# Optimization experiments

Measured on AMD Instinct MI355X. Metric: run time of the kernel, lower is better.

Reference implementation:

```python
import jax, jax.numpy as jnp
import numpy as np

B, TED, G, N, E, MD, NOISE = 10000, 512, 64, 2000, 64000, 15, 128
PAC = 10
PACDIM = (TED + NOISE) * PAC  # 6400
D0, D1 = 1024, 512


def _linear_params(k, fan_in, fan_out):
    kw, kb = jax.random.split(k)
    lim = 1.0 / np.sqrt(fan_in)
    w = jax.random.uniform(kw, (fan_in, fan_out), minval=-lim, maxval=lim, dtype=jnp.float32)
    b = jax.random.uniform(kb, (fan_out,), minval=-lim, maxval=lim, dtype=jnp.float32)
    return w, b


def setup_inputs() -> dict:
    key = jax.random.key(0)
    ks = jax.random.split(key, 12)
    inp = {
        'input_': jax.random.normal(ks[0], (B, TED), dtype=jnp.float32),
        'graphs_x': jax.random.normal(ks[1], (G, N, 1), dtype=jnp.float32),
        'edge_index': jax.random.randint(ks[2], (G, 2, E), 0, N, dtype=jnp.int32),
        'graph_ids': jax.random.randint(ks[3], (B,), 0, G, dtype=jnp.int32),
        'chain': jax.random.normal(ks[4], (B, 1), dtype=jnp.float32),
        'metadata': jax.random.normal(ks[5], (B, MD), dtype=jnp.float32),
    }
    inp['gcn_w'], inp['gcn_b'] = _linear_params(ks[6], 1, 1)
    inp['meta_w'], inp['meta_b'] = _linear_params(ks[7], 1 + MD, 32)
    inp['gme_w'], inp['gme_b'] = _linear_params(ks[8], N + 32, NOISE)
    inp['seq_w0'], inp['seq_b0'] = _linear_params(ks[9], PACDIM, D0)
    inp['seq_w1'], inp['seq_b1'] = _linear_params(ks[10], D0, D1)
    inp['seq_w2'], inp['seq_b2'] = _linear_params(ks[11], D1, 1)
    return inp


def _gcn_one(x, ei, gcn_w, gcn_b):
    # GCNConv(1,1) with self-loops and symmetric normalization.
    loops = jnp.arange(N, dtype=ei.dtype)
    src = jnp.concatenate([ei[0], loops])
    dst = jnp.concatenate([ei[1], loops])
    deg = jax.ops.segment_sum(jnp.ones_like(src, dtype=x.dtype), dst, num_segments=N)
    dinv = jax.lax.rsqrt(deg)  # deg >= 1 due to self-loops
    norm = dinv[src] * dinv[dst]  # [E+N]
    xw = x @ gcn_w  # [N,1]
    msg = xw[src] * norm[:, None]
    out = jax.ops.segment_sum(msg, dst, num_segments=N) + gcn_b
    return out.reshape(-1)  # flatten -> [N]


def reference(input_, graphs_x, edge_index, graph_ids, chain, metadata,
              gcn_w, gcn_b, meta_w, meta_b, gme_w, gme_b,
              seq_w0, seq_b0, seq_w1, seq_b1, seq_w2, seq_b2):
    # per-unique-graph GCN, vectorized over G graphs
    gcn_out = jax.vmap(lambda x, ei: _gcn_one(x, ei, gcn_w, gcn_b))(graphs_x, edge_index)  # [G,N]
    graph_emb = gcn_out[graph_ids]  # gather: [B,N]
    all_meta = jnp.concatenate([chain, metadata], axis=1)  # [B,1+MD]
    meta_emb = jax.nn.relu(all_meta @ meta_w + meta_b)  # [B,32]
    noise = jnp.concatenate([graph_emb, meta_emb], axis=1) @ gme_w + gme_b  # [B,NOISE]
    h = jnp.concatenate([input_, noise], axis=1).reshape(-1, PACDIM)  # [B/PAC, PACDIM]
    h = jax.nn.leaky_relu(h @ seq_w0 + seq_b0, 0.2)  # dropout omitted (eval mode)
    h = jax.nn.leaky_relu(h @ seq_w1 + seq_b1, 0.2)
    return h @ seq_w2 + seq_b2  # [B/PAC, 1]
```

## Files before the change

### kernel.cpp

```cpp
#include <hip/hip_runtime.h>

typedef __bf16 bf16_t;
typedef __bf16 bf16x4 __attribute__((ext_vector_type(4)));
typedef __bf16 bf16x8 __attribute__((ext_vector_type(8)));
typedef float floatx4 __attribute__((ext_vector_type(4)));

#define G_GRAPHS 64
#define N_NODES 2000
#define N_EDGES 64000
#define BATCH 10000
#define TED_ 512
#define NOISE_ 128
#define PACDIM_ 6400
#define D0_ 1024
#define D1_ 512
#define MROWS 1000
#define ESPLIT 8
#define EPB (N_EDGES / ESPLIT)
#define MSPLIT 8
#define EPB_MSG (N_EDGES / MSPLIT)
#define S0 8

#define DEG_BLKS 512
#define PACK_BLKS 1250
#define W0T_BLKS 6400
#define W1T_BLKS 512

__device__ __forceinline__ void glds16(const void* g, void* l) {
    __builtin_amdgcn_global_load_lds(
        (__attribute__((address_space(1))) void*)(g),
        (__attribute__((address_space(3))) void*)(l), 16, 0, 0);
}

__global__ __launch_bounds__(256) void prep_kernel(
    const int* __restrict__ edge_index, float* __restrict__ degs_part,
    const float* __restrict__ in, bf16_t* __restrict__ A,
    const float* __restrict__ W0, bf16_t* __restrict__ W0t,
    const float* __restrict__ W1, bf16_t* __restrict__ W1t)
{
    __shared__ float h[N_NODES];
    __shared__ float t[32][33];
    const int b = blockIdx.x, tid = threadIdx.x;
    if (b < DEG_BLKS) {
        const int s = b & 7, g = b >> 3;
        for (int n = tid; n < N_NODES; n += 256) h[n] = 0.f;
        __syncthreads();
        const int4* d4 = (const int4*)(edge_index + (size_t)g * 2 * N_EDGES
                                       + N_EDGES + s * EPB);
        for (int e = tid; e < EPB / 4; e += 256) {
            int4 v = d4[e];
            atomicAdd(&h[v.x], 1.0f); atomicAdd(&h[v.y], 1.0f);
            atomicAdd(&h[v.z], 1.0f); atomicAdd(&h[v.w], 1.0f);
        }
        __syncthreads();
        float* dp = degs_part + ((size_t)g * ESPLIT + s) * N_NODES;
        for (int n = tid; n < N_NODES; n += 256) dp[n] = h[n];
        return;
    }
    if (b < DEG_BLKS + PACK_BLKS) {
        int base = (b - DEG_BLKS) * 1024;
        for (int u = 0; u < 4; u++) {
            int idx = base + u * 256 + tid;
            float4 v = ((const float4*)in)[idx];
            int bb = idx >> 7;
            int c = (idx & 127) << 2;
            int r = bb / 10, slot = bb - r * 10;
            bf16x4 o = { (bf16_t)v.x, (bf16_t)v.y, (bf16_t)v.z, (bf16_t)v.w };
            *(bf16x4*)(A + (size_t)r * PACDIM_ + slot * 640 + c) = o;
        }
        return;
    }
    const float* W; bf16_t* Wt; int Rr, Cc, c0, r0;
    if (b < DEG_BLKS + PACK_BLKS + W0T_BLKS) {
        int tile = b - (DEG_BLKS + PACK_BLKS);
        W = W0; Wt = W0t; Rr = PACDIM_; Cc = D0_;
        c0 = (tile & 31) << 5; r0 = (tile >> 5) << 5;
    } else {
        int tile = b - (DEG_BLKS + PACK_BLKS + W0T_BLKS);
        W = W1; Wt = W1t; Rr = D0_; Cc = D1_;
        c0 = (tile & 15) << 5; r0 = (tile >> 4) << 5;
    }
    int tx = tid & 31, ty = tid >> 5;
    for (int yy = ty; yy < 32; yy += 8)
        t[yy][tx] = W[(size_t)(r0 + yy) * Cc + c0 + tx];
    __syncthreads();
    for (int yy = ty; yy < 32; yy += 8)
        Wt[(size_t)(c0 + yy) * Rr + r0 + tx] = (bf16_t)t[tx][yy];
}

__global__ __launch_bounds__(512) void msg_kernel(
    const float* __restrict__ graphs_x, const int* __restrict__ edge_index,
    const float* __restrict__ degs_part, float* __restrict__ outs_part)
{
    __shared__ float ys[N_NODES];
    __shared__ float dvl[N_NODES];
    __shared__ float oh[N_NODES];
    const int g = blockIdx.y, s = blockIdx.x, tid = threadIdx.x;
    const float* xg = graphs_x + (size_t)g * N_NODES;
    const float* dgp = degs_part + (size_t)g * ESPLIT * N_NODES;
    for (int n = tid; n < N_NODES; n += 512) {
        float d = 1.0f;
        for (int p = 0; p < ESPLIT; p++) d += dgp[(size_t)p * N_NODES + n];
        float dv = rsqrtf(d);
        dvl[n] = dv;
        ys[n] = xg[n] * dv;
        oh[n] = 0.f;
    }
    __syncthreads();
    const int* src = edge_index + (size_t)g * 2 * N_EDGES + s * EPB_MSG;
    const int2* s2 = (const int2*)src;
    const int2* d2 = (const int2*)(src + N_EDGES);
    for (int e = tid; e < EPB_MSG / 2; e += 512) {
        int2 sv = s2[e], dd = d2[e];
        atomicAdd(&oh[dd.x], ys[sv.x] * dvl[dd.x]);
        atomicAdd(&oh[dd.y], ys[sv.y] * dvl[dd.y]);
    }
    __syncthreads();
    float* op = outs_part + ((size_t)g * MSPLIT + s) * N_NODES;
    for (int n = tid; n < N_NODES; n += 512) op[n] = oh[n];
}

__global__ __launch_bounds__(512) void gnoise_kernel(
    const float* __restrict__ graphs_x, const float* __restrict__ degs_part,
    const float* __restrict__ outs_part,
    const float* __restrict__ gcn_w, const float* __restrict__ gcn_b,
    const float* __restrict__ gme_w, float* __restrict__ gnoise_p)
{
    __shared__ float of[500];
    __shared__ float part[4][128];
    const int s = blockIdx.x, g = blockIdx.y, tid = threadIdx.x;
    const int nBase = s * 500;
    const float w = gcn_w[0], bb = gcn_b[0];
    const float* dgp = degs_part + (size_t)g * ESPLIT * N_NODES;
    const float* otp = outs_part + (size_t)g * MSPLIT * N_NODES;
    for (int n = tid; n < 500; n += 512) {
        int gn = nBase + n;
        float d = 1.0f, o = 0.f;
        for (int p = 0; p < ESPLIT; p++) d += dgp[(size_t)p * N_NODES + gn];
        for (int p = 0; p < MSPLIT; p++) o += otp[(size_t)p * N_NODES + gn];
        of[n] = w * (o + graphs_x[(size_t)g * N_NODES + gn] / d) + bb;
    }
    __syncthreads();
    const int j = tid & 127, ch = tid >> 7;
    float acc = 0.f;
    const int n0 = ch * 125;
    for (int n = n0; n < n0 + 125; n++)
        acc += of[n] * gme_w[(size_t)(nBase + n) * 128 + j];
    part[ch][j] = acc;
    __syncthreads();
    if (tid < 128)
        gnoise_p[((size_t)g * 4 + s) * 128 + tid] =
            part[0][tid] + part[1][tid] + part[2][tid] + part[3][tid];
}

__global__ __launch_bounds__(256) void meta_kernel(
    const float* __restrict__ chain, const float* __restrict__ metadata,
    const int* __restrict__ graph_ids,
    const float* __restrict__ meta_w, const float* __restrict__ meta_b,
    const float* __restrict__ gme_w, const float* __restrict__ gme_b,
    const float* __restrict__ gnoise_p, bf16_t* __restrict__ A)
{
    int wid = (blockIdx.x * 256 + threadIdx.x) >> 6;
    int lane = threadIdx.x & 63;
    if (wid >= BATCH) return;
    const int b = wid;
    float me = 0.f;
    if (lane < 32) {
        me = meta_b[lane] + chain[b] * meta_w[lane];
        for (int i = 1; i < 16; i++)
            me += metadata[(size_t)b * 15 + (i - 1)] * meta_w[(size_t)i * 32 + lane];
        me = me > 0.f ? me : 0.f;
    }
    const int gid = graph_ids[b];
    const float* gp = gnoise_p + (size_t)gid * 4 * 128;
    const int j1 = lane, j2 = lane + 64;
    float n1 = gme_b[j1] + gp[j1] + gp[128 + j1] + gp[256 + j1] + gp[384 + j1];
    float n2 = gme_b[j2] + gp[j2] + gp[128 + j2] + gp[256 + j2] + gp[384 + j2];
    for (int k = 0; k < 32; k++) {
        float mk = __shfl(me, k, 64);
        const float* wrow = gme_w + (size_t)(N_NODES + k) * 128;
        n1 += mk * wrow[j1];
        n2 += mk * wrow[j2];
    }
    int r = b / 10, slot = b - r * 10;
    bf16_t* dp = A + (size_t)r * PACDIM_ + slot * 640 + TED_;
    dp[j1] = (bf16_t)n1;
    dp[j2] = (bf16_t)n2;
}

__global__ __launch_bounds__(256) void gemm_bt_splitk_kernel(
    const bf16_t* __restrict__ A,
    const bf16_t* __restrict__ Bt,
    float* __restrict__ P,
    int M, int N, int K, int KS, int zbits, int xbits, int Mp)
{
    __shared__ __align__(16) bf16_t As[2][128 * 32];
    __shared__ __align__(16) bf16_t Bs[2][128 * 32];
    const int tid = threadIdx.x;
    const int wave = tid >> 6;
    const int lane = tid & 63;
    const int id = blockIdx.x;
    const int z = id & ((1 << zbits) - 1);
    const int xt = (id >> zbits) & ((1 << xbits) - 1);
    const int yt = id >> (zbits + xbits);
    const int mBase = yt * 128;
    const int nBase = xt * 128;
    const int wm = (wave & 1) * 64;
    const int wn = (wave >> 1) * 64;

    floatx4 acc[4][4] = {};

    const int rA0 = tid >> 2;
    const int g4 = tid & 3;
    const int f4 = (rA0 >> 1) & 3;
    const int k8 = (g4 ^ f4) * 8;
    int gm0 = mBase + rA0;      if (gm0 > M - 1) gm0 = M - 1;
    int gm1 = mBase + 64 + rA0; if (gm1 > M - 1) gm1 = M - 1;
    const bf16_t* aP0 = A + (size_t)gm0 * K + k8;
    const bf16_t* aP1 = A + (size_t)gm1 * K + k8;
    const bf16_t* bP0 = Bt + (size_t)(nBase + rA0) * K + k8;
    const bf16_t* bP1 = Bt + (size_t)(nBase + 64 + rA0) * K + k8;

    const int q4 = lane >> 4;
    const int mr = lane & 15;
    const int kq = ((q4 ^ ((mr >> 1) & 3)) * 8);
    int aOff[4], bOff[4];
    for (int i = 0; i < 4; i++) aOff[i] = (wm + i * 16 + mr) * 32 + kq;
    for (int j = 0; j < 4; j++) bOff[j] = (wn + j * 16 + mr) * 32 + kq;

    const int nIter = KS >> 5;
    const int kc = z * KS;
    {
        char* lA = (char*)(&As[0][0]) + wave * 1024;
        char* lB = (char*)(&Bs[0][0]) + wave * 1024;
        glds16(aP0 + kc, lA);
        glds16(aP1 + kc, lA + 4096);
        glds16(bP0 + kc, lB);
        glds16(bP1 + kc, lB + 4096);
    }
    __syncthreads();
    for (int t = 0; t < nIter; ++t) {
        const int cur = t & 1;
        if (t + 1 < nIter) {
            const int kn = kc + (t + 1) * 32;
            char* lA = (char*)(&As[cur ^ 1][0]) + wave * 1024;
            char* lB = (char*)(&Bs[cur ^ 1][0]) + wave * 1024;
            glds16(aP0 + kn, lA);
            glds16(aP1 + kn, lA + 4096);
            glds16(bP0 + kn, lB);
            glds16(bP1 + kn, lB + 4096);
        }
        const bf16_t* aB = &As[cur][0];
        const bf16_t* bB = &Bs[cur][0];
        bf16x8 af[4], bfr[4];
        for (int i = 0; i < 4; i++) af[i] = *(const bf16x8*)(aB + aOff[i]);
        for (int j = 0; j < 4; j++) bfr[j] = *(const bf16x8*)(bB + bOff[j]);
        for (int i = 0; i < 4; i++)
            for (int j = 0; j < 4; j++)
                acc[i][j] = __builtin_amdgcn_mfma_f32_16x16x32_bf16(
                    af[i], bfr[j], acc[i][j], 0, 0, 0);
        __syncthreads();
    }

    float* Pz = P + (size_t)z * Mp * N;
    const int rq = (lane >> 4) * 4;
    const int cn = lane & 15;
    for (int j = 0; j < 4; j++) {
        int col = nBase + wn + j * 16 + cn;
        for (int i = 0; i < 4; i++)
            for (int r = 0; r < 4; r++) {
                int rowm = mBase + wm + i * 16 + rq + r;
                Pz[(size_t)rowm * N + col] = acc[i][j][r];
            }
    }
}

__global__ __launch_bounds__(256) void reduce_bias_leaky_kernel(
    const float* __restrict__ P, const float* __restrict__ bias,
    bf16_t* __restrict__ C, int M, int N, int Mp, int S,
    const float* __restrict__ b2, float* __restrict__ outp)
{
    if (blockIdx.x == 0 && threadIdx.x < MROWS / 4) {
        float bb2 = b2[0];
        ((float4*)outp)[threadIdx.x] = make_float4(bb2, bb2, bb2, bb2);
    }
    int idx = blockIdx.x * 256 + threadIdx.x;
    int total = M * (N >> 2);
    if (idx >= total) return;
    int nv = N >> 2;
    int r = idx / nv, c4 = (idx - r * nv) << 2;
    size_t off = (size_t)r * N + c4;
    size_t stride = (size_t)Mp * N;
    float4 v = *(const float4*)(P + off);
    for (int s = 1; s < S; s++) {
        float4 u = *(const float4*)(P + s * stride + off);
        v.x += u.x; v.y += u.y; v.z += u.z; v.w += u.w;
    }
    const float4 bv = *(const float4*)(bias + c4);
    v.x += bv.x; v.y += bv.y; v.z += bv.z; v.w += bv.w;
    v.x = v.x > 0.f ? v.x : 0.2f * v.x;
    v.y = v.y > 0.f ? v.y : 0.2f * v.y;
    v.z = v.z > 0.f ? v.z : 0.2f * v.z;
    v.w = v.w > 0.f ? v.w : 0.2f * v.w;
    bf16x4 o = { (bf16_t)v.x, (bf16_t)v.y, (bf16_t)v.z, (bf16_t)v.w };
    *(bf16x4*)(C + off) = o;
}

__global__ __launch_bounds__(256) void gemm1_final_kernel(
    const bf16_t* __restrict__ A,
    const bf16_t* __restrict__ Bt,
    const float* __restrict__ b1, const float* __restrict__ w2,
    float* __restrict__ outp)
{
    __shared__ __align__(16) bf16_t As[2][128 * 32];
    __shared__ __align__(16) bf16_t Bs[2][128 * 32];
    const int K = D0_;
    const int tid = threadIdx.x;
    const int wave = tid >> 6;
    const int lane = tid & 63;
    const int xt = blockIdx.x & 3;
    const int yt = blockIdx.x >> 2;
    const int mBase = yt * 128;
    const int nBase = xt * 128;
    const int wm = (wave & 1) * 64;
    const int wn = (wave >> 1) * 64;

    floatx4 acc[4][4] = {};

    const int rA0 = tid >> 2;
    const int g4 = tid & 3;
    const int f4 = (rA0 >> 1) & 3;
    const int k8 = (g4 ^ f4) * 8;
    int gm0 = mBase + rA0;      if (gm0 > MROWS - 1) gm0 = MROWS - 1;
    int gm1 = mBase + 64 + rA0; if (gm1 > MROWS - 1) gm1 = MROWS - 1;
    const bf16_t* aP0 = A + (size_t)gm0 * K + k8;
    const bf16_t* aP1 = A + (size_t)gm1 * K + k8;
    const bf16_t* bP0 = Bt + (size_t)(nBase + rA0) * K + k8;
    const bf16_t* bP1 = Bt + (size_t)(nBase + 64 + rA0) * K + k8;

    const int q4 = lane >> 4;
    const int mr = lane & 15;
    const int kq = ((q4 ^ ((mr >> 1) & 3)) * 8);
    int aOff[4], bOff[4];
    for (int i = 0; i < 4; i++) aOff[i] = (wm + i * 16 + mr) * 32 + kq;
    for (int j = 0; j < 4; j++) bOff[j] = (wn + j * 16 + mr) * 32 + kq;

    const int nIter = K >> 5;
    {
        char* lA = (char*)(&As[0][0]) + wave * 1024;
        char* lB = (char*)(&Bs[0][0]) + wave * 1024;
        glds16(aP0, lA);
        glds16(aP1, lA + 4096);
        glds16(bP0, lB);
        glds16(bP1, lB + 4096);
    }
    __syncthreads();
    for (int t = 0; t < nIter; ++t) {
        const int cur = t & 1;
        if (t + 1 < nIter) {
            const int kn = (t + 1) * 32;
            char* lA = (char*)(&As[cur ^ 1][0]) + wave * 1024;
            char* lB = (char*)(&Bs[cur ^ 1][0]) + wave * 1024;
            glds16(aP0 + kn, lA);
            glds16(aP1 + kn, lA + 4096);
            glds16(bP0 + kn, lB);
            glds16(bP1 + kn, lB + 4096);
        }
        const bf16_t* aB = &As[cur][0];
        const bf16_t* bB = &Bs[cur][0];
        bf16x8 af[4], bfr[4];
        for (int i = 0; i < 4; i++) af[i] = *(const bf16x8*)(aB + aOff[i]);
        for (int j = 0; j < 4; j++) bfr[j] = *(const bf16x8*)(bB + bOff[j]);
        for (int i = 0; i < 4; i++)
            for (int j = 0; j < 4; j++)
                acc[i][j] = __builtin_amdgcn_mfma_f32_16x16x32_bf16(
                    af[i], bfr[j], acc[i][j], 0, 0, 0);
        __syncthreads();
    }

    const int cn = lane & 15;
    float b1v[4], w2v[4];
    for (int j = 0; j < 4; j++) {
        int col = nBase + wn + j * 16 + cn;
        b1v[j] = b1[col];
        w2v[j] = w2[col];
    }
    for (int i = 0; i < 4; i++) {
        for (int r = 0; r < 4; r++) {
            float part = 0.f;
            for (int j = 0; j < 4; j++) {
                float v = acc[i][j][r] + b1v[j];
                v = v > 0.f ? v : 0.2f * v;
                part += v * w2v[j];
            }
            for (int off = 8; off; off >>= 1) part += __shfl_xor(part, off, 16);
            if (cn == 0) {
                int rowm = mBase + wm + i * 16 + q4 * 4 + r;
                if (rowm < MROWS) atomicAdd(&outp[rowm], part);
            }
        }
    }
}

extern "C" void kernel_launch(void* const* d_in, const int* in_sizes, int n_in,
                              void* d_out, int out_size, void* d_ws, size_t ws_size,
                              hipStream_t stream)
{
    const float* input_    = (const float*)d_in[0];
    const float* graphs_x  = (const float*)d_in[1];
    const int*   edge_idx  = (const int*)  d_in[2];
    const int*   graph_ids = (const int*)  d_in[3];
    const float* chain     = (const float*)d_in[4];
    const float* metadata  = (const float*)d_in[5];
    const float* gcn_w     = (const float*)d_in[6];
    const float* gcn_b     = (const float*)d_in[7];
    const float* meta_w    = (const float*)d_in[8];
    const float* meta_b    = (const float*)d_in[9];
    const float* gme_w     = (const float*)d_in[10];
    const float* gme_b     = (const float*)d_in[11];
    const float* seq_w0    = (const float*)d_in[12];
    const float* seq_b0    = (const float*)d_in[13];
    const float* seq_w1    = (const float*)d_in[14];
    const float* seq_b1    = (const float*)d_in[15];
    const float* seq_w2    = (const float*)d_in[16];
    const float* seq_b2    = (const float*)d_in[17];
    float* out = (float*)d_out;

    char* ws = (char*)d_ws;
    float*  degs_part = (float*)(ws + 0);
    float*  outs_part = (float*)(ws + 4096000);
    float*  gnoise_p  = (float*)(ws + 8192000);
    bf16_t* Abuf      = (bf16_t*)(ws + 8323072);
    bf16_t* W0t       = (bf16_t*)(ws + 21123072);
    bf16_t* W1t       = (bf16_t*)(ws + 34230272);
    bf16_t* H1        = (bf16_t*)(ws + 35278848);
    float*  P         = (float*)(ws + 37326848);

    prep_kernel<<<DEG_BLKS + PACK_BLKS + W0T_BLKS + W1T_BLKS, 256, 0, stream>>>(
        edge_idx, degs_part, input_, Abuf, seq_w0, W0t, seq_w1, W1t);
    msg_kernel<<<dim3(MSPLIT, G_GRAPHS), 512, 0, stream>>>(
        graphs_x, edge_idx, degs_part, outs_part);
    gnoise_kernel<<<dim3(4, G_GRAPHS), 512, 0, stream>>>(
        graphs_x, degs_part, outs_part, gcn_w, gcn_b, gme_w, gnoise_p);
    meta_kernel<<<2500, 256, 0, stream>>>(
        chain, metadata, graph_ids, meta_w, meta_b, gme_w, gme_b,
        gnoise_p, Abuf);

    gemm_bt_splitk_kernel<<<512, 256, 0, stream>>>(
        Abuf, W0t, P, MROWS, D0_, PACDIM_, PACDIM_ / S0, 3, 3, 1024);
    reduce_bias_leaky_kernel<<<(MROWS * D0_ / 4 + 255) / 256, 256, 0, stream>>>(
        P, seq_b0, H1, MROWS, D0_, 1024, S0, seq_b2, out);

    gemm1_final_kernel<<<32, 256, 0, stream>>>(
        H1, W1t, seq_b1, seq_w2, out);
}
```

Baseline: 265.1 us.

## Fuse GCN stages into cooperative kernel and widen weight transpose tiles

The degree count, message passing and graph-noise projection are merged into one cooperative kernel that uses grid-wide syncs in place of three separate launches. Degree histogramming moves out of prep_kernel. Separately, the weight transpose/convert now works on 64x64 tiles with float4 loads and bf16x8 stores, replacing 32x32 tiles with scalar accesses. Risks: cooperative launch needs all 512 blocks co-resident, the grid syncs add cost, and the graph kernel now runs serially before prep instead of sharing its launch.

```diff
diff --git a/kernel.cpp b/kernel.cpp
--- a/kernel.cpp
+++ b/kernel.cpp
@@ -1,4 +1,7 @@
 #include <hip/hip_runtime.h>
+#include <hip/hip_cooperative_groups.h>
+
+namespace cg = cooperative_groups;
 
 typedef __bf16 bf16_t;
 typedef __bf16 bf16x4 __attribute__((ext_vector_type(4)));
@@ -17,14 +20,11 @@
 #define MROWS 1000
 #define ESPLIT 8
 #define EPB (N_EDGES / ESPLIT)
-#define MSPLIT 8
-#define EPB_MSG (N_EDGES / MSPLIT)
 #define S0 8
 
-#define DEG_BLKS 512
 #define PACK_BLKS 1250
-#define W0T_BLKS 6400
-#define W1T_BLKS 512
+#define W0T_BLKS 1600
+#define W1T_BLKS 128
 
 __device__ __forceinline__ void glds16(const void* g, void* l) {
     __builtin_amdgcn_global_load_lds(
@@ -32,33 +32,105 @@
         (__attribute__((address_space(3))) void*)(l), 16, 0, 0);
 }
 
+__global__ __launch_bounds__(512) void graph_kernel(
+    const float* __restrict__ graphs_x, const int* __restrict__ edge_index,
+    float* __restrict__ degs_part, float* __restrict__ outs_part,
+    const float* __restrict__ gcn_w, const float* __restrict__ gcn_b,
+    const float* __restrict__ gme_w, float* __restrict__ gnoise_p)
+{
+    __shared__ __align__(16) float sm[3 * N_NODES];
+    cg::grid_group grid = cg::this_grid();
+    const int b = blockIdx.x, tid = threadIdx.x;
+    const int s = b & 7, g = b >> 3;
+
+    {
+        float* h = sm;
+        for (int n = tid; n < N_NODES; n += 512) h[n] = 0.f;
+        __syncthreads();
+        const int4* d4 = (const int4*)(edge_index + (size_t)g * 2 * N_EDGES
+                                       + N_EDGES + s * EPB);
+        for (int e = tid; e < EPB / 4; e += 512) {
+            int4 v = d4[e];
+            atomicAdd(&h[v.x], 1.0f); atomicAdd(&h[v.y], 1.0f);
+            atomicAdd(&h[v.z], 1.0f); atomicAdd(&h[v.w], 1.0f);
+        }
+        __syncthreads();
+        float* dp = degs_part + ((size_t)g * ESPLIT + s) * N_NODES;
+        for (int n = tid; n < N_NODES; n += 512) dp[n] = h[n];
+    }
+    __threadfence();
+    grid.sync();
+
+    {
+        float* ys  = sm;
+        float* dvl = sm + N_NODES;
+        float* oh  = sm + 2 * N_NODES;
+        const float* xg = graphs_x + (size_t)g * N_NODES;
+        const float* dgp = degs_part + (size_t)g * ESPLIT * N_NODES;
+        for (int n = tid; n < N_NODES; n += 512) {
+            float d = 1.0f;
+            for (int p = 0; p < ESPLIT; p++) d += dgp[(size_t)p * N_NODES + n];
+            float dv = rsqrtf(d);
+            dvl[n] = dv;
+            ys[n] = xg[n] * dv;
+            oh[n] = 0.f;
+        }
+        __syncthreads();
+        const int* src = edge_index + (size_t)g * 2 * N_EDGES + s * EPB;
+        const int2* s2 = (const int2*)src;
+        const int2* d2 = (const int2*)(src + N_EDGES);
+        for (int e = tid; e < EPB / 2; e += 512) {
+            int2 sv = s2[e], dd = d2[e];
+            atomicAdd(&oh[dd.x], ys[sv.x] * dvl[dd.x]);
+            atomicAdd(&oh[dd.y], ys[sv.y] * dvl[dd.y]);
+        }
+        __syncthreads();
+        float* op = outs_part + ((size_t)g * ESPLIT + s) * N_NODES;
+        for (int n = tid; n < N_NODES; n += 512) op[n] = oh[n];
+    }
+    __threadfence();
+    grid.sync();
+
+    if (b < 256) {
+        const int s3 = b & 3, g3 = b >> 2;
+        float* of = sm;
+        float (*part)[128] = (float(*)[128])(sm + 512);
+        const int nBase = s3 * 500;
+        const float w = gcn_w[0], bb = gcn_b[0];
+        const float* dgp = degs_part + (size_t)g3 * ESPLIT * N_NODES;
+        const float* otp = outs_part + (size_t)g3 * ESPLIT * N_NODES;
+        for (int n = tid; n < 500; n += 512) {
+            int gn = nBase + n;
+            float d = 1.0f, o = 0.f;
+            for (int p = 0; p < ESPLIT; p++) {
+                d += dgp[(size_t)p * N_NODES + gn];
+                o += otp[(size_t)p * N_NODES + gn];
+            }
+            of[n] = w * (o + graphs_x[(size_t)g3 * N_NODES + gn] / d) + bb;
+        }
+        __syncthreads();
+        const int j = tid & 127, ch = tid >> 7;
+        float acc = 0.f;
+        const int n0 = ch * 125;
+        for (int n = n0; n < n0 + 125; n++)
+            acc += of[n] * gme_w[(size_t)(nBase + n) * 128 + j];
+        part[ch][j] = acc;
+        __syncthreads();
+        if (tid < 128)
+            gnoise_p[((size_t)g3 * 4 + s3) * 128 + tid] =
+                part[0][tid] + part[1][tid] + part[2][tid] + part[3][tid];
+    }
+}
+
 __global__ __launch_bounds__(256) void prep_kernel(
-    const int* __restrict__ edge_index, float* __restrict__ degs_part,
     const float* __restrict__ in, bf16_t* __restrict__ A,
     const float* __restrict__ W0, bf16_t* __restrict__ W0t,
     const float* __restrict__ W1, bf16_t* __restrict__ W1t)
 {
-    __shared__ float h[N_NODES];
-    __shared__ float t[32][33];
+    __shared__ float t[64][67];
     const int b = blockIdx.x, tid = threadIdx.x;
-    if (b < DEG_BLKS) {
-        const int s = b & 7, g = b >> 3;
-        for (int n = tid; n < N_NODES; n += 256) h[n] = 0.f;
-        __syncthreads();
-        const int4* d4 = (const int4*)(edge_index + (size_t)g * 2 * N_EDGES
-                                       + N_EDGES + s * EPB);
-        for (int e = tid; e < EPB / 4; e += 256) {
-            int4 v = d4[e];
-            atomicAdd(&h[v.x], 1.0f); atomicAdd(&h[v.y], 1.0f);
-            atomicAdd(&h[v.z], 1.0f); atomicAdd(&h[v.w], 1.0f);
-        }
-        __syncthreads();
-        float* dp = degs_part + ((size_t)g * ESPLIT + s) * N_NODES;
-        for (int n = tid; n < N_NODES; n += 256) dp[n] = h[n];
-        return;
-    }
-    if (b < DEG_BLKS + PACK_BLKS) {
-        int base = (b - DEG_BLKS) * 1024;
+    if (b < PACK_BLKS) {
+        int base = b * 1024;
         for (int u = 0; u < 4; u++) {
             int idx = base + u * 256 + tid;
             float4 v = ((const float4*)in)[idx];
@@ -70,87 +142,30 @@
         }
         return;
     }
-    const float* W; bf16_t* Wt; int Rr, Cc, c0, r0;
-    if (b < DEG_BLKS + PACK_BLKS + W0T_BLKS) {
-        int tile = b - (DEG_BLKS + PACK_BLKS);
+    const float* W; bf16_t* Wt; int Rr, Cc, r0, c0;
+    if (b < PACK_BLKS + W0T_BLKS) {
+        int tile = b - PACK_BLKS;
         W = W0; Wt = W0t; Rr = PACDIM_; Cc = D0_;
-        c0 = (tile & 31) << 5; r0 = (tile >> 5) << 5;
+        r0 = (tile >> 4) << 6; c0 = (tile & 15) << 6;
     } else {
-        int tile = b - (DEG_BLKS + PACK_BLKS + W0T_BLKS);
+        int tile = b - (PACK_BLKS + W0T_BLKS);
         W = W1; Wt = W1t; Rr = D0_; Cc = D1_;
-        c0 = (tile & 15) << 5; r0 = (tile >> 4) << 5;
-    }
-    int tx = tid & 31, ty = tid >> 5;
-    for (int yy = ty; yy < 32; yy += 8)
-        t[yy][tx] = W[(size_t)(r0 + yy) * Cc + c0 + tx];
+        r0 = (tile >> 3) << 6; c0 = (tile & 7) << 6;
+    }
+    for (int u = 0; u < 4; u++) {
+        int idx = u * 256 + tid;
+        int r = idx >> 4, c4 = (idx & 15) << 2;
+        float4 v = *(const float4*)(W + (size_t)(r0 + r) * Cc + c0 + c4);
+        t[r][c4] = v.x; t[r][c4 + 1] = v.y; t[r][c4 + 2] = v.z; t[r][c4 + 3] = v.w;
+    }
     __syncthreads();
-    for (int yy = ty; yy < 32; yy += 8)
-        Wt[(size_t)(c0 + yy) * Rr + r0 + tx] = (bf16_t)t[tx][yy];
-}
-
-__global__ __launch_bounds__(512) void msg_kernel(
-    const float* __restrict__ graphs_x, const int* __restrict__ edge_index,
-    const float* __restrict__ degs_part, float* __restrict__ outs_part)
-{
-    __shared__ float ys[N_NODES];
-    __shared__ float dvl[N_NODES];
-    __shared__ float oh[N_NODES];
-    const int g = blockIdx.y, s = blockIdx.x, tid = threadIdx.x;
-    const float* xg = graphs_x + (size_t)g * N_NODES;
-    const float* dgp = degs_part + (size_t)g * ESPLIT * N_NODES;
-    for (int n = tid; n < N_NODES; n += 512) {
-        float d = 1.0f;
-        for (int p = 0; p < ESPLIT; p++) d += dgp[(size_t)p * N_NODES + n];
-        float dv = rsqrtf(d);
-        dvl[n] = dv;
-        ys[n] = xg[n] * dv;
-        oh[n] = 0.f;
-    }
-    __syncthreads();
-    const int* src = edge_index + (size_t)g * 2 * N_EDGES + s * EPB_MSG;
-    const int2* s2 = (const int2*)src;
-    const int2* d2 = (const int2*)(src + N_EDGES);
-    for (int e = tid; e < EPB_MSG / 2; e += 512) {
-        int2 sv = s2[e], dd = d2[e];
-        atomicAdd(&oh[dd.x], ys[sv.x] * dvl[dd.x]);
-        atomicAdd(&oh[dd.y], ys[sv.y] * dvl[dd.y]);
-    }
-    __syncthreads();
-    float* op = outs_part + ((size_t)g * MSPLIT + s) * N_NODES;
-    for (int n = tid; n < N_NODES; n += 512) op[n] = oh[n];
-}
-
-__global__ __launch_bounds__(512) void gnoise_kernel(
-    const float* __restrict__ graphs_x, const float* __restrict__ degs_part,
-    const float* __restrict__ outs_part,
-    const float* __restrict__ gcn_w, const float* __restrict__ gcn_b,
-    const float* __restrict__ gme_w, float* __restrict__ gnoise_p)
-{
-    __shared__ float of[500];
-    __shared__ float part[4][128];
-    const int s = blockIdx.x, g = blockIdx.y, tid = threadIdx.x;
-    const int nBase = s * 500;
-    const float w = gcn_w[0], bb = gcn_b[0];
-    const float* dgp = degs_part + (size_t)g * ESPLIT * N_NODES;
-    const float* otp = outs_part + (size_t)g * MSPLIT * N_NODES;
-    for (int n = tid; n < 500; n += 512) {
-        int gn = nBase + n;
-        float d = 1.0f, o = 0.f;
-        for (int p = 0; p < ESPLIT; p++) d += dgp[(size_t)p * N_NODES + gn];
-        for (int p = 0; p < MSPLIT; p++) o += otp[(size_t)p * N_NODES + gn];
-        of[n] = w * (o + graphs_x[(size_t)g * N_NODES + gn] / d) + bb;
-    }
-    __syncthreads();
-    const int j = tid & 127, ch = tid >> 7;
-    float acc = 0.f;
-    const int n0 = ch * 125;
-    for (int n = n0; n < n0 + 125; n++)
-        acc += of[n] * gme_w[(size_t)(nBase + n) * 128 + j];
-    part[ch][j] = acc;
-    __syncthreads();
-    if (tid < 128)
-        gnoise_p[((size_t)g * 4 + s) * 128 + tid] =
-            part[0][tid] + part[1][tid] + part[2][tid] + part[3][tid];
+    for (int u = 0; u < 2; u++) {
+        int widx = u * 256 + tid;
+        int c = widx >> 3, seg = widx & 7;
+        bf16x8 o;
+        for (int jj = 0; jj < 8; jj++) o[jj] = (bf16_t)t[seg * 8 + jj][c];
+        *(bf16x8*)(Wt + (size_t)(c0 + c) * Rr + r0 + seg * 8) = o;
+    }
 }
 
 __global__ __launch_bounds__(256) void meta_kernel(
@@ -436,12 +451,15 @@
     bf16_t* H1        = (bf16_t*)(ws + 35278848);
     float*  P         = (float*)(ws + 37326848);
 
-    prep_kernel<<<DEG_BLKS + PACK_BLKS + W0T_BLKS + W1T_BLKS, 256, 0, stream>>>(
-        edge_idx, degs_part, input_, Abuf, seq_w0, W0t, seq_w1, W1t);
-    msg_kernel<<<dim3(MSPLIT, G_GRAPHS), 512, 0, stream>>>(
-        graphs_x, edge_idx, degs_part, outs_part);
-    gnoise_kernel<<<dim3(4, G_GRAPHS), 512, 0, stream>>>(
-        graphs_x, degs_part, outs_part, gcn_w, gcn_b, gme_w, gnoise_p);
+    void* gargs[] = {
+        (void*)&graphs_x, (void*)&edge_idx, (void*)&degs_part, (void*)&outs_part,
+        (void*)&gcn_w, (void*)&gcn_b, (void*)&gme_w, (void*)&gnoise_p
+    };
+    hipLaunchCooperativeKernel(graph_kernel, dim3(512), dim3(512), gargs, 0, stream);
+
+    prep_kernel<<<PACK_BLKS + W0T_BLKS + W1T_BLKS, 256, 0, stream>>>(
+        input_, Abuf, seq_w0, W0t, seq_w1, W1t);
+
     meta_kernel<<<2500, 256, 0, stream>>>(
         chain, metadata, graph_ids, meta_w, meta_b, gme_w, gme_b,
         gnoise_p, Abuf);
```

Result: slower. 537.8 us (+102.9%).
